# Kernel tuning notes

Measured on AMD Instinct MI355X. Metric: run time of the kernel, lower is better.

## Reference

```python
import jax, jax.numpy as jnp
import numpy as np

B, T, S0 = 8, 4, 4096
D_MODEL, H, D, R, RANK = 2048, 16, 128, 64, 512
C = D - R  # content dim = 64


def _rope(x, positions):
    # x: [B, H, T, R]; rotate-half style RoPE as in the torch module
    half = x.shape[-1] // 2
    inv_freq = 1.0 / (10000.0 ** (jnp.arange(half, dtype=jnp.float32) / half))
    freqs = positions.astype(jnp.float32)[:, None] * inv_freq[None, :]  # [T, half]
    cos = jnp.cos(freqs)[None, None].astype(x.dtype)
    sin = jnp.sin(freqs)[None, None].astype(x.dtype)
    x1, x2 = x[..., :half], x[..., half:]
    return jnp.concatenate([x1 * cos - x2 * sin, x1 * sin + x2 * cos], axis=-1)


def setup_inputs() -> dict:
    key = jax.random.key(0)
    ks = jax.random.split(key, 9)
    s = 0.02
    return {
        "x": jax.random.normal(ks[0], (B, T, D_MODEL), jnp.float32),
        "cache_c_kv": jax.random.normal(ks[1], (B, S0, RANK), jnp.float32),
        "cache_k_rope": jax.random.normal(ks[2], (B, S0, H, R), jnp.float32),
        "w_q": jax.random.normal(ks[3], (D_MODEL, H * C), jnp.float32) * s,
        "w_q_rope": jax.random.normal(ks[4], (D_MODEL, H * R), jnp.float32) * s,
        "w_kv_down": jax.random.normal(ks[5], (D_MODEL, RANK), jnp.float32) * s,
        "w_kv_up": jax.random.normal(ks[6], (RANK, H * D), jnp.float32) * s,
        "w_k_rope": jax.random.normal(ks[7], (D_MODEL, H * R), jnp.float32) * s,
        "w_out": jax.random.normal(ks[8], (H * D, D_MODEL), jnp.float32) * s,
    }


def reference(x, cache_c_kv, cache_k_rope, w_q, w_q_rope, w_kv_down, w_kv_up, w_k_rope, w_out):
    cache_len = cache_c_kv.shape[1]
    positions = jnp.arange(cache_len, cache_len + T)

    # queries
    q_content = (x @ w_q).reshape(B, T, H, C).transpose(0, 2, 1, 3)        # [B,H,T,C]
    q_rope = (x @ w_q_rope).reshape(B, T, H, R).transpose(0, 2, 1, 3)      # [B,H,T,R]
    q_rope = _rope(q_rope, positions)
    q = jnp.concatenate([q_content, q_rope], axis=-1)                       # [B,H,T,D]

    # new compressed kv + rope keys, append to cache
    c_kv_new = x @ w_kv_down                                                # [B,T,RANK]
    k_rope_new = (x @ w_k_rope).reshape(B, T, H, R).transpose(0, 2, 1, 3)
    k_rope_new = _rope(k_rope_new, positions).transpose(0, 2, 1, 3)         # [B,T,H,R]
    c_kv = jnp.concatenate([cache_c_kv, c_kv_new], axis=1)                  # [B,S,RANK]
    k_rope = jnp.concatenate([cache_k_rope, k_rope_new], axis=1)            # [B,S,H,R]

    # decompress full cache every step (the expensive MLA pattern)
    S = c_kv.shape[1]
    kv = (c_kv @ w_kv_up).reshape(B, S, H, D)                               # [B,S,H,D]
    k_content = kv[..., :C].transpose(0, 2, 1, 3)                           # [B,H,S,C]
    v = kv.transpose(0, 2, 1, 3)                                            # [B,H,S,D]
    k = jnp.concatenate([k_content, k_rope.transpose(0, 2, 1, 3)], axis=-1) # [B,H,S,D]

    # kv_cache present => is_prefill False => no causal mask (faithful to source)
    scale = 1.0 / jnp.sqrt(jnp.asarray(D, dtype=q.dtype))
    scores = jnp.einsum('bhtd,bhsd->bhts', q, k) * scale
    attn = jax.nn.softmax(scores, axis=-1)
    out = jnp.einsum('bhts,bhsd->bhtd', attn, v)                            # [B,H,T,D]
    out = out.transpose(0, 2, 1, 3).reshape(B, T, H * D)
    return out @ w_out                                                       # [B,T,D_MODEL]
```

## Files before the change

### kernel.cpp

```cpp
#include <hip/hip_runtime.h>
#include <hip/hip_fp16.h>
#include <cmath>

#define BB 8
#define TT 4
#define HH 16
#define DDIM 128
#define RRDIM 64
#define CCDIM 64
#define RANKC 512
#define DMODEL 2048
#define S0C 4096
#define NQ 64
#define HD 2048
#define NACT 3584
#define NSC 65
#define NG 17
#define SPAD 4160
#define SCALE_ATT 0.08838834764831845f

typedef __attribute__((ext_vector_type(8))) short bf16x8;
typedef __attribute__((ext_vector_type(4))) float f32x4;
typedef unsigned short ushortT;

#define AIDX(row, kk) ((row)*132 + (((row)>>2)<<2) + (kk))

static __device__ __forceinline__ unsigned short f2bf(float x) {
  unsigned u = __float_as_uint(x);
  u += 0x7FFFu + ((u >> 16) & 1u);
  return (unsigned short)(u >> 16);
}
static __device__ __forceinline__ unsigned pk2(float a, float b) {
  return (unsigned)f2bf(a) | ((unsigned)f2bf(b) << 16);
}

__global__ __launch_bounds__(256) void k_front(const float* __restrict__ A,
                                               const float* __restrict__ w0,
                                               const float* __restrict__ w1,
                                               const float* __restrict__ w2,
                                               const float* __restrict__ w3,
                                               const float* __restrict__ cckv,
                                               float* __restrict__ part,
                                               ushortT* __restrict__ ckvB,
                                               ushortT* __restrict__ ckvT,
                                               float* __restrict__ rctab) {
  __shared__ float shf[4352];
  const int tid = threadIdx.x;
  const int bx = blockIdx.x;
  if (bx < 448) {
    const int cb = bx % 28;
    const int k0 = (bx / 28) * 128;
    const float* W; int N, lc0, off;
    if (cb < 8)       { W = w0; N = 1024; lc0 = cb * 128;        off = 0; }
    else if (cb < 16) { W = w1; N = 1024; lc0 = (cb - 8) * 128;  off = 1024; }
    else if (cb < 20) { W = w2; N = 512;  lc0 = (cb - 16) * 128; off = 2048; }
    else              { W = w3; N = 1024; lc0 = (cb - 20) * 128; off = 2560; }
    {
      const int row = tid >> 3;
      const int kseg = (tid & 7) * 16;
      const float4* s4 = reinterpret_cast<const float4*>(A + (size_t)row * DMODEL + k0 + kseg);
      float4 v0 = s4[0], v1 = s4[1], v2 = s4[2], v3 = s4[3];
      *reinterpret_cast<float4*>(&shf[AIDX(row, kseg)])      = v0;
      *reinterpret_cast<float4*>(&shf[AIDX(row, kseg + 4)])  = v1;
      *reinterpret_cast<float4*>(&shf[AIDX(row, kseg + 8)])  = v2;
      *reinterpret_cast<float4*>(&shf[AIDX(row, kseg + 12)]) = v3;
    }
    __syncthreads();
    const int cg = tid & 31;
    const int rg = tid >> 5;
    float acc[4][4];
    #pragma unroll
    for (int r = 0; r < 4; ++r)
      #pragma unroll
      for (int c = 0; c < 4; ++c) acc[r][c] = 0.f;
    #pragma unroll 4
    for (int kk = 0; kk < 128; ++kk) {
      const float4 w4 = *reinterpret_cast<const float4*>(W + (size_t)(k0 + kk) * N + lc0 + cg * 4);
      const float wv[4] = {w4.x, w4.y, w4.z, w4.w};
      #pragma unroll
      for (int r = 0; r < 4; ++r) {
        const float av = shf[AIDX(rg * 4 + r, kk)];
        #pragma unroll
        for (int c = 0; c < 4; ++c) acc[r][c] = fmaf(av, wv[c], acc[r][c]);
      }
    }
    #pragma unroll
    for (int r = 0; r < 4; ++r) {
      float4 o = make_float4(acc[r][0], acc[r][1], acc[r][2], acc[r][3]);
      *reinterpret_cast<float4*>(part + ((size_t)(bx / 28) * 32 + rg * 4 + r) * NACT + off + lc0 + cg * 4) = o;
    }
  } else if (bx < 960) {
    ushortT* tlds = reinterpret_cast<ushortT*>(shf);
    const int idx = bx - 448;
    const int b = idx >> 6, c = idx & 63;
    const float* src = cckv + ((size_t)b * S0C + c * 64) * RANKC;
    ushortT* dstB = ckvB + ((size_t)(b * NSC + c) * 64) * RANKC;
    ushortT* dstT = ckvT + ((size_t)(b * NSC + c) * RANKC) * 64;
    const int s = tid >> 2, rq = tid & 3;
    const int rloc = tid >> 1, shalf = (tid & 1) * 32;
    for (int slab = 0; slab < 4; ++slab) {
      const int r0 = slab * 128;
      unsigned pk_arr[16];
      #pragma unroll
      for (int i = 0; i < 8; ++i) {
        const float4 v = *reinterpret_cast<const float4*>(src + (size_t)s * RANKC + r0 + rq * 32 + i * 4);
        pk_arr[2 * i]     = pk2(v.x, v.y);
        pk_arr[2 * i + 1] = pk2(v.z, v.w);
        *reinterpret_cast<uint2*>(&tlds[s * 136 + rq * 32 + i * 4]) =
            make_uint2(pk_arr[2 * i], pk_arr[2 * i + 1]);
      }
      {
        uint4* db = reinterpret_cast<uint4*>(dstB + (size_t)s * RANKC + r0 + rq * 32);
        db[0] = make_uint4(pk_arr[0], pk_arr[1], pk_arr[2], pk_arr[3]);
        db[1] = make_uint4(pk_arr[4], pk_arr[5], pk_arr[6], pk_arr[7]);
        db[2] = make_uint4(pk_arr[8], pk_arr[9], pk_arr[10], pk_arr[11]);
        db[3] = make_uint4(pk_arr[12], pk_arr[13], pk_arr[14], pk_arr[15]);
      }
      __syncthreads();
      unsigned pkv[16];
      #pragma unroll
      for (int k = 0; k < 16; ++k) {
        const unsigned t0 = tlds[(shalf + 2 * k)     * 136 + rloc];
        const unsigned t1 = tlds[(shalf + 2 * k + 1) * 136 + rloc];
        pkv[k] = t0 | (t1 << 16);
      }
      uint4* d = reinterpret_cast<uint4*>(dstT + ((size_t)(r0 + rloc)) * 64 + shalf);
      d[0] = make_uint4(pkv[0], pkv[1], pkv[2], pkv[3]);
      d[1] = make_uint4(pkv[4], pkv[5], pkv[6], pkv[7]);
      d[2] = make_uint4(pkv[8], pkv[9], pkv[10], pkv[11]);
      d[3] = make_uint4(pkv[12], pkv[13], pkv[14], pkv[15]);
      __syncthreads();
    }
  } else {
    const int b = bx - 960;
    const uint4 z = make_uint4(0, 0, 0, 0);
    uint4* p = reinterpret_cast<uint4*>(ckvT + ((size_t)(b * NSC + 64) * RANKC) * 64);
    for (int i = tid; i < 4096; i += 256) p[i] = z;
    uint4* q = reinterpret_cast<uint4*>(ckvB + (((size_t)(b * NSC + 64) * 64) + 4) * RANKC);
    for (int i = tid; i < 3840; i += 256) q[i] = z;
    if (bx == 960 && tid < 128) {
      const int t = tid >> 5, j = tid & 31;
      const double fr = (double)(S0C + t) * pow(10000.0, -(double)j / 32.0);
      rctab[t * 32 + j]       = (float)cos(fr);
      rctab[128 + t * 32 + j] = (float)sin(fr);
    }
  }
}

__global__ __launch_bounds__(256) void k_mid(const float* __restrict__ part0,
                                             const float* __restrict__ cache_kr,
                                             const float* __restrict__ wup,
                                             const float* __restrict__ rctab,
                                             ushortT* __restrict__ qlat,
                                             ushortT* __restrict__ ckvB,
                                             ushortT* __restrict__ ckvT,
                                             __half* __restrict__ rs) {
  __shared__ float smid[2176];
  const int tid = threadIdx.x;
  const int bx = blockIdx.x;
  if (bx < 1152) {
    const int bh = bx / 9, sy = bx % 9;
    const int b = bh >> 4, h = bh & 15;
    float* raw_q = smid;
    float* raw_k = smid + 256;
    float* qr_l  = smid + 512;
    float* kr_l  = smid + 768;
    {
      const int t = tid >> 6, j = tid & 63;
      const size_t rowoff = (size_t)(b * TT + t) * NACT;
      float sq = 0.f, sk = 0.f;
      #pragma unroll 4
      for (int ks = 0; ks < 16; ++ks) {
        const float* pp = part0 + (size_t)ks * (32 * NACT) + rowoff;
        sq += pp[1024 + h * 64 + j];
        sk += pp[2560 + h * 64 + j];
      }
      raw_q[t * 64 + j] = sq;
      raw_k[t * 64 + j] = sk;
    }
    __syncthreads();
    {
      const int t = tid >> 6, j = tid & 63;
      const int j2 = j & 31;
      const float cs = rctab[t * 32 + j2];
      const float sn = rctab[128 + t * 32 + j2];
      const float qa = raw_q[t * 64 + j], qp = raw_q[t * 64 + (j ^ 32)];
      const float ka = raw_k[t * 64 + j], kp = raw_k[t * 64 + (j ^ 32)];
      float qv, kv;
      if (j < 32) { qv = qa * cs - qp * sn; kv = ka * cs - kp * sn; }
      else        { qv = qp * sn + qa * cs; kv = kp * sn + ka * cs; }
      qr_l[t * 64 + j] = qv * SCALE_ATT;
      kr_l[t * 64 + j] = kv;
    }
    __syncthreads();
    const int ql = tid & 3;
    float4 qf[4][4];
    #pragma unroll
    for (int t = 0; t < 4; ++t)
      #pragma unroll
      for (int u = 0; u < 4; ++u)
        qf[t][u] = *reinterpret_cast<const float4*>(&qr_l[t * 64 + ql * 16 + u * 4]);
    const int s0 = sy * 512;
    #pragma unroll 2
    for (int pass = 0; pass < 8; ++pass) {
      const int s = s0 + pass * 64 + (tid >> 2);
      if (s < 4100) {
        float p[4] = {0.f, 0.f, 0.f, 0.f};
        const float* krow = (s < S0C)
            ? cache_kr + (((size_t)b * S0C + s) * HH + h) * RRDIM
            : &kr_l[(s - S0C) * 64];
        #pragma unroll
        for (int u = 0; u < 4; ++u) {
          const float4 kv = *reinterpret_cast<const float4*>(krow + ql * 16 + u * 4);
          #pragma unroll
          for (int t = 0; t < 4; ++t)
            p[t] += kv.x * qf[t][u].x + kv.y * qf[t][u].y
                  + kv.z * qf[t][u].z + kv.w * qf[t][u].w;
        }
        #pragma unroll
        for (int t = 0; t < 4; ++t) {
          p[t] += __shfl_xor(p[t], 1, 4);
          p[t] += __shfl_xor(p[t], 2, 4);
        }
        rs[((size_t)bh * 4 + ql) * SPAD + s] = __float2half(p[ql]);
      }
    }
  } else if (bx < 1216) {
    const int lx = bx - 1152;
    const int h = lx & 15;
    const int r0 = (lx >> 4) * 128;
    float* a_s = smid;
    {
      const int bt = tid >> 3;
      const int c8 = (tid & 7) * 8;
      float v[8] = {0.f,0.f,0.f,0.f,0.f,0.f,0.f,0.f};
      #pragma unroll 4
      for (int ks = 0; ks < 16; ++ks) {
        const float4* pp = reinterpret_cast<const float4*>(
            part0 + (size_t)ks * (32 * NACT) + (size_t)bt * NACT + h * CCDIM + c8);
        const float4 x0 = pp[0], x1 = pp[1];
        v[0]+=x0.x; v[1]+=x0.y; v[2]+=x0.z; v[3]+=x0.w;
        v[4]+=x1.x; v[5]+=x1.y; v[6]+=x1.z; v[7]+=x1.w;
      }
      #pragma unroll
      for (int u = 0; u < 8; ++u) a_s[bt * 68 + c8 + u] = v[u];
    }
    __syncthreads();
    const int r = tid & 127;
    const int bth = tid >> 7;
    const float* wrow = wup + (size_t)(r0 + r) * HD + h * DDIM;
    float4 wreg[16];
    #pragma unroll
    for (int u = 0; u < 16; ++u)
      wreg[u] = *reinterpret_cast<const float4*>(wrow + u * 4);
    float acc[16];
    #pragma unroll
    for (int i = 0; i < 16; ++i) acc[i] = 0.f;
    #pragma unroll
    for (int u = 0; u < 16; ++u) {
      #pragma unroll
      for (int i = 0; i < 16; ++i) {
        const float4 av = *reinterpret_cast<const float4*>(&a_s[(bth * 16 + i) * 68 + u * 4]);
        acc[i] = fmaf(av.x, wreg[u].x, acc[i]);
        acc[i] = fmaf(av.y, wreg[u].y, acc[i]);
        acc[i] = fmaf(av.z, wreg[u].z, acc[i]);
        acc[i] = fmaf(av.w, wreg[u].w, acc[i]);
      }
    }
    #pragma unroll
    for (int i = 0; i < 16; ++i) {
      const int bt = bth * 16 + i;
      const int b = bt >> 2, t = bt & 3;
      qlat[((size_t)(b * NQ) + h * TT + t) * RANKC + r0 + r] = f2bf(acc[i]);
    }
  } else {
    const int g = (bx - 1216) * 256 + tid;
    const int r = g & 511;
    const int bt = g >> 9;
    const int b = bt >> 2, t = bt & 3;
    float s = 0.f;
    #pragma unroll 4
    for (int ks = 0; ks < 16; ++ks)
      s += part0[(size_t)ks * (32 * NACT) + (size_t)bt * NACT + 2048 + r];
    const ushortT bv = f2bf(s);
    ckvB[(((size_t)(b * NSC + 64) * 64) + t) * RANKC + r] = bv;
    ckvT[(((size_t)(b * NSC + 64) * RANKC) + r) * 64 + t] = bv;
  }
}

__global__ __launch_bounds__(256) void k_score(
    const ushortT* __restrict__ ckvB, const ushortT* __restrict__ qlat,
    const __half* __restrict__ rs, float* __restrict__ ml,
    ushortT* __restrict__ Pg) {
  __shared__ ushortT PL[64 * 72];
  const int tid = threadIdx.x;
  const int wv = tid >> 6;
  const int lane = tid & 63;
  const int lm = lane & 15, lg = lane >> 4;
  const int b = blockIdx.x, chunk = blockIdx.y;
  const int qbase = wv * 16;
  const int scnt = (chunk < 64) ? 64 : TT;
  const ushortT* bsrc = ckvB + ((size_t)(b * NSC + chunk) * 64) * RANKC;

  const ushortT* qrow = qlat + ((size_t)b * NQ + qbase + lm) * RANKC + lg * 8;
  bf16x8 qa[16];
  #pragma unroll
  for (int ks = 0; ks < 16; ++ks)
    qa[ks] = *reinterpret_cast<const bf16x8*>(qrow + ks * 32);

  f32x4 acc[4];
  #pragma unroll
  for (int st = 0; st < 4; ++st) acc[st] = (f32x4){0.f, 0.f, 0.f, 0.f};
  #pragma unroll
  for (int ks = 0; ks < 16; ++ks) {
    #pragma unroll
    for (int st = 0; st < 4; ++st) {
      const bf16x8 bf = *reinterpret_cast<const bf16x8*>(
          bsrc + (size_t)(st * 16 + lm) * RANKC + ks * 32 + lg * 8);
      acc[st] = __builtin_amdgcn_mfma_f32_16x16x32_bf16(qa[ks], bf, acc[st], 0, 0, 0);
    }
  }

  #pragma unroll
  for (int reg = 0; reg < 4; ++reg) {
    const int qi = qbase + lg * 4 + reg;
    const __half* rp = rs + (((size_t)(b * HH) + (qi >> 2)) * TT + (qi & 3)) * SPAD + chunk * 64;
    float vvv[4];
    float mx = -1e30f;
    #pragma unroll
    for (int st = 0; st < 4; ++st) {
      const int sl = st * 16 + lm;
      const float val = (sl < scnt)
          ? fmaf(acc[st][reg], SCALE_ATT, __half2float(rp[sl]))
          : -1e30f;
      vvv[st] = val;
      mx = fmaxf(mx, val);
    }
    #pragma unroll
    for (int off = 1; off < 16; off <<= 1) mx = fmaxf(mx, __shfl_xor(mx, off, 16));
    float sum = 0.f;
    #pragma unroll
    for (int st = 0; st < 4; ++st) {
      const float p = __expf(vvv[st] - mx);
      vvv[st] = p;
      sum += p;
    }
    #pragma unroll
    for (int off = 1; off < 16; off <<= 1) sum += __shfl_xor(sum, off, 16);
    #pragma unroll
    for (int st = 0; st < 4; ++st)
      PL[(qbase + lg * 4 + reg) * 72 + st * 16 + lm] = f2bf(vvv[st]);
    if (lm == 0) {
      const size_t mb = (((size_t)b * NSC + chunk) * NQ + qi) * 2;
      ml[mb] = mx; ml[mb + 1] = sum;
    }
  }
  __syncthreads();
  {
    const int row = tid >> 2, seg = (tid & 3) * 16;
    const uint4* sp = reinterpret_cast<const uint4*>(&PL[row * 72 + seg]);
    uint4* dp = reinterpret_cast<uint4*>(
        Pg + ((size_t)(b * NSC + chunk) * NQ + row) * 64 + seg);
    dp[0] = sp[0]; dp[1] = sp[1];
  }
}

__global__ __launch_bounds__(256) void k_pv(
    const ushortT* __restrict__ ckvT, const ushortT* __restrict__ Pg,
    const float* __restrict__ ml, float* __restrict__ olat,
    float* __restrict__ mlg) {
  const int tid = threadIdx.x;
  const int wv = tid >> 6;
  const int lane = tid & 63;
  const int lm = lane & 15, lg = lane >> 4;
  const int b = blockIdx.x, g = blockIdx.y, rg = blockIdx.z;
  const int qbase = wv * 16;
  const int nc = (g < 16) ? 4 : 1;
  const int c0 = (g < 16) ? g * 4 : 64;

  float m_cl = -1e30f, l_cl = 0.f;
  if (lg < nc) {
    const size_t mb = (((size_t)b * NSC + c0 + lg) * NQ + qbase + lm) * 2;
    m_cl = ml[mb]; l_cl = ml[mb + 1];
  }
  float mg = fmaxf(m_cl, __shfl_xor(m_cl, 16));
  mg = fmaxf(mg, __shfl_xor(mg, 32));
  const float wgt = (lg < nc) ? __expf(m_cl - mg) : 0.f;
  float la = l_cl * wgt;
  la += __shfl_xor(la, 16);
  la += __shfl_xor(la, 32);
  if (rg == 0 && lg == 0) {
    const size_t gb = (((size_t)b * NG + g) * NQ + qbase + lm) * 2;
    mlg[gb] = mg; mlg[gb + 1] = la;
  }
  float wf[4][4];
  #pragma unroll
  for (int c = 0; c < 4; ++c)
    #pragma unroll
    for (int reg = 0; reg < 4; ++reg)
      wf[c][reg] = __shfl(wgt, c * 16 + lg * 4 + reg);

  f32x4 OACC[8];
  #pragma unroll
  for (int nt = 0; nt < 8; ++nt) OACC[nt] = (f32x4){0.f, 0.f, 0.f, 0.f};

  for (int c = 0; c < nc; ++c) {
    const ushortT* pb = Pg + ((size_t)(b * NSC + c0 + c) * NQ + qbase + lm) * 64 + lg * 8;
    const bf16x8 pa0 = *reinterpret_cast<const bf16x8*>(pb);
    const bf16x8 pa1 = *reinterpret_cast<const bf16x8*>(pb + 32);
    const ushortT* vb = ckvT + (((size_t)(b * NSC + c0 + c) * RANKC) + rg * 128 + lm) * 64 + lg * 8;
    f32x4 a2[8];
    #pragma unroll
    for (int nt = 0; nt < 8; ++nt) a2[nt] = (f32x4){0.f, 0.f, 0.f, 0.f};
    #pragma unroll
    for (int nt = 0; nt < 8; ++nt) {
      const bf16x8 b0 = *reinterpret_cast<const bf16x8*>(vb + (size_t)nt * 16 * 64);
      const bf16x8 b1 = *reinterpret_cast<const bf16x8*>(vb + (size_t)nt * 16 * 64 + 32);
      a2[nt] = __builtin_amdgcn_mfma_f32_16x16x32_bf16(pa0, b0, a2[nt], 0, 0, 0);
      a2[nt] = __builtin_amdgcn_mfma_f32_16x16x32_bf16(pa1, b1, a2[nt], 0, 0, 0);
    }
    const f32x4 wv4 = {wf[c][0], wf[c][1], wf[c][2], wf[c][3]};
    #pragma unroll
    for (int nt = 0; nt < 8; ++nt) OACC[nt] += wv4 * a2[nt];
  }

  const size_t obase = ((size_t)(b * NG + g) * NQ) * RANKC;
  #pragma unroll
  for (int nt = 0; nt < 8; ++nt)
    #pragma unroll
    for (int reg = 0; reg < 4; ++reg)
      olat[obase + (size_t)(qbase + lg * 4 + reg) * RANKC + rg * 128 + nt * 16 + lm] = OACC[nt][reg];
}

__global__ __launch_bounds__(512) void k_combF(const float* __restrict__ mlg,
                                               const float* __restrict__ olat,
                                               const float* __restrict__ wup,
                                               float* __restrict__ ohead,
                                               float* __restrict__ out) {
  __shared__ float wrow[4][20];
  __shared__ float att_lds[4][516];
  __shared__ float red[4][4][32][4];
  const int h = blockIdx.x, b = blockIdx.y;
  const int tid = threadIdx.x;
  {
    const int t = tid >> 7, col = tid & 127;
    out[(size_t)(b * TT + t) * HD + h * DDIM + col] = 0.f;
  }
  const int wave = tid >> 6;
  const int i = wave >> 1;
  const int rhalf = wave & 1;
  const int rl = tid & 63;
  const int qi = h * TT + i;
  float m1 = -1e30f, l1 = 0.f;
  if (rl < NG) {
    const size_t base = (((size_t)b * NG + rl) * NQ + qi) * 2;
    m1 = mlg[base]; l1 = mlg[base + 1];
  }
  float M = m1;
  #pragma unroll
  for (int off = 1; off < 64; off <<= 1) M = fmaxf(M, __shfl_xor(M, off));
  float L = (rl < NG) ? l1 * __expf(m1 - M) : 0.f;
  #pragma unroll
  for (int off = 1; off < 64; off <<= 1) L += __shfl_xor(L, off);
  const float invL = 1.0f / L;
  if (rl < NG) wrow[i][rl] = __expf(m1 - M) * invL;
  __syncthreads();
  const int r0 = rhalf * 256 + rl * 4;
  {
    float o0 = 0.f, o1 = 0.f, o2 = 0.f, o3 = 0.f;
    for (int c = 0; c < NG; ++c) {
      const float w = wrow[i][c];
      const float4 v = *reinterpret_cast<const float4*>(
          olat + (((size_t)b * NG + c) * NQ + qi) * RANKC + r0);
      o0 = fmaf(v.x, w, o0); o1 = fmaf(v.y, w, o1);
      o2 = fmaf(v.z, w, o2); o3 = fmaf(v.w, w, o3);
    }
    *reinterpret_cast<float4*>(&att_lds[i][r0]) = make_float4(o0, o1, o2, o3);
  }
  __syncthreads();
  const int t = tid >> 7;
  const int rq = (tid >> 5) & 3;
  const int c4 = tid & 31;
  const float* wb = wup + (size_t)h * DDIM + c4 * 4;
  float a0 = 0.f, a1 = 0.f, a2 = 0.f, a3 = 0.f;
  const int rbeg = rq * 128;
  #pragma unroll 4
  for (int rr = 0; rr < 128; ++rr) {
    const int r = rbeg + rr;
    const float4 w4 = *reinterpret_cast<const float4*>(wb + (size_t)r * HD);
    const float a = att_lds[t][r];
    a0 = fmaf(a, w4.x, a0); a1 = fmaf(a, w4.y, a1);
    a2 = fmaf(a, w4.z, a2); a3 = fmaf(a, w4.w, a3);
  }
  *reinterpret_cast<float4*>(&red[rq][t][c4][0]) = make_float4(a0, a1, a2, a3);
  __syncthreads();
  if (tid < 128) {
    const int t2 = tid >> 5, c42 = tid & 31;
    float4 s = make_float4(0.f, 0.f, 0.f, 0.f);
    #pragma unroll
    for (int q = 0; q < 4; ++q) {
      const float4 v = *reinterpret_cast<const float4*>(&red[q][t2][c42][0]);
      s.x += v.x; s.y += v.y; s.z += v.z; s.w += v.w;
    }
    *reinterpret_cast<float4*>(&ohead[(size_t)(b * TT + t2) * HD + h * DDIM + c42 * 4]) = s;
  }
}

__global__ __launch_bounds__(256) void k_projA(const float* __restrict__ A,
                                               const float* __restrict__ W,
                                               float* __restrict__ out) {
  __shared__ float a_lds[4352];
  const int tid = threadIdx.x;
  const int c0 = blockIdx.x * 128;
  const int k0 = blockIdx.y * 128;
  {
    const int row = tid >> 3;
    const int kseg = (tid & 7) * 16;
    const float4* s4 = reinterpret_cast<const float4*>(A + (size_t)row * DMODEL + k0 + kseg);
    float4 v0 = s4[0], v1 = s4[1], v2 = s4[2], v3 = s4[3];
    *reinterpret_cast<float4*>(&a_lds[AIDX(row, kseg)])      = v0;
    *reinterpret_cast<float4*>(&a_lds[AIDX(row, kseg + 4)])  = v1;
    *reinterpret_cast<float4*>(&a_lds[AIDX(row, kseg + 8)])  = v2;
    *reinterpret_cast<float4*>(&a_lds[AIDX(row, kseg + 12)]) = v3;
  }
  __syncthreads();
  const int cg = tid & 31;
  const int rg = tid >> 5;
  float acc[4][4];
  #pragma unroll
  for (int r = 0; r < 4; ++r)
    #pragma unroll
    for (int c = 0; c < 4; ++c) acc[r][c] = 0.f;
  #pragma unroll 4
  for (int kk = 0; kk < 128; ++kk) {
    const float4 w4 = *reinterpret_cast<const float4*>(W + (size_t)(k0 + kk) * HD + c0 + cg * 4);
    const float wv[4] = {w4.x, w4.y, w4.z, w4.w};
    #pragma unroll
    for (int r = 0; r < 4; ++r) {
      const float av = a_lds[AIDX(rg * 4 + r, kk)];
      #pragma unroll
      for (int c = 0; c < 4; ++c) acc[r][c] = fmaf(av, wv[c], acc[r][c]);
    }
  }
  #pragma unroll
  for (int r = 0; r < 4; ++r)
    #pragma unroll
    for (int c = 0; c < 4; ++c)
      unsafeAtomicAdd(&out[(size_t)(rg * 4 + r) * HD + c0 + cg * 4 + c], acc[r][c]);
}

extern "C" void kernel_launch(void* const* d_in, const int* in_sizes, int n_in,
                              void* d_out, int out_size, void* d_ws, size_t ws_size,
                              hipStream_t stream) {
  const float* x     = (const float*)d_in[0];
  const float* cckv  = (const float*)d_in[1];
  const float* ckr   = (const float*)d_in[2];
  const float* w_q   = (const float*)d_in[3];
  const float* w_qr  = (const float*)d_in[4];
  const float* w_kvd = (const float*)d_in[5];
  const float* w_kvu = (const float*)d_in[6];
  const float* w_kr  = (const float*)d_in[7];
  const float* w_out = (const float*)d_in[8];
  float* out = (float*)d_out;
  float* ws = (float*)d_ws;

  size_t off = 0;
  ushortT* qlat   = (ushortT*)(ws + off); off += 131072;
  float* mlb      = ws + off; off += (size_t)BB * NSC * NQ * 2;
  float* mlgb     = ws + off; off += (size_t)BB * NG * NQ * 2;
  float* ohead    = ws + off; off += 65536;
  float* rctab    = ws + off; off += 256;
  __half* rsb     = (__half*)(ws + off); off += 1064960;
  ushortT* ckvB   = (ushortT*)(ws + off); off += 8519680;
  ushortT* ckvT   = (ushortT*)(ws + off); off += 8519680;
  ushortT* Pgb    = (ushortT*)(ws + off); off += 1064960;
  float* regB  = ws + off;
  float* part0 = regB;
  float* olat  = regB;

  k_front<<<dim3(968), 256, 0, stream>>>(x, w_q, w_qr, w_kvd, w_kr, cckv, part0, ckvB, ckvT, rctab);
  k_mid<<<dim3(1280), 256, 0, stream>>>(part0, ckr, w_kvu, rctab, qlat, ckvB, ckvT, rsb);
  k_score<<<dim3(BB, NSC), 256, 0, stream>>>(ckvB, qlat, rsb, mlb, Pgb);
  k_pv<<<dim3(BB, NG, 4), 256, 0, stream>>>(ckvT, Pgb, mlb, olat, mlgb);
  k_combF<<<dim3(16, 8), 512, 0, stream>>>(mlgb, olat, w_kvu, ohead, out);
  k_projA<<<dim3(16, 16), 256, 0, stream>>>(ohead, w_out, out);
}
```

Before: 210.1 us.

## Raise parallelism across MLA stages with atomic split-K reductions and finer grids

The front projection now accumulates its K-split partial sums with atomic adds into a zeroed activation buffer instead of writing 16 partial slabs that later stages summed. The cache conversion work is split into one block per 128-column slab, and the mid, pv and combine kernels are launched with more, smaller blocks; the combine kernel splits the rank dimension across blocks and accumulates into ohead atomically. The aim is to fill more CUs and cut redundant partial-sum reads, at the cost of extra memsets, atomic traffic and non-deterministic summation order.

```diff
diff --git a/kernel.cpp b/kernel.cpp
--- a/kernel.cpp
+++ b/kernel.cpp
@@ -40,7 +40,7 @@
                                                const float* __restrict__ w2,
                                                const float* __restrict__ w3,
                                                const float* __restrict__ cckv,
-                                               float* __restrict__ part,
+                                               float* __restrict__ act,
                                                ushortT* __restrict__ ckvB,
                                                ushortT* __restrict__ ckvT,
                                                float* __restrict__ rctab) {
@@ -85,60 +85,57 @@
       }
     }
     #pragma unroll
-    for (int r = 0; r < 4; ++r) {
-      float4 o = make_float4(acc[r][0], acc[r][1], acc[r][2], acc[r][3]);
-      *reinterpret_cast<float4*>(part + ((size_t)(bx / 28) * 32 + rg * 4 + r) * NACT + off + lc0 + cg * 4) = o;
-    }
-  } else if (bx < 960) {
+    for (int r = 0; r < 4; ++r)
+      #pragma unroll
+      for (int c = 0; c < 4; ++c)
+        unsafeAtomicAdd(&act[(size_t)(rg * 4 + r) * NACT + off + lc0 + cg * 4 + c], acc[r][c]);
+  } else if (bx < 2496) {
     ushortT* tlds = reinterpret_cast<ushortT*>(shf);
     const int idx = bx - 448;
-    const int b = idx >> 6, c = idx & 63;
+    const int b = idx >> 8, c = (idx >> 2) & 63, slab = idx & 3;
+    const int r0 = slab * 128;
     const float* src = cckv + ((size_t)b * S0C + c * 64) * RANKC;
     ushortT* dstB = ckvB + ((size_t)(b * NSC + c) * 64) * RANKC;
     ushortT* dstT = ckvT + ((size_t)(b * NSC + c) * RANKC) * 64;
     const int s = tid >> 2, rq = tid & 3;
     const int rloc = tid >> 1, shalf = (tid & 1) * 32;
-    for (int slab = 0; slab < 4; ++slab) {
-      const int r0 = slab * 128;
-      unsigned pk_arr[16];
-      #pragma unroll
-      for (int i = 0; i < 8; ++i) {
-        const float4 v = *reinterpret_cast<const float4*>(src + (size_t)s * RANKC + r0 + rq * 32 + i * 4);
-        pk_arr[2 * i]     = pk2(v.x, v.y);
-        pk_arr[2 * i + 1] = pk2(v.z, v.w);
-        *reinterpret_cast<uint2*>(&tlds[s * 136 + rq * 32 + i * 4]) =
-            make_uint2(pk_arr[2 * i], pk_arr[2 * i + 1]);
-      }
-      {
-        uint4* db = reinterpret_cast<uint4*>(dstB + (size_t)s * RANKC + r0 + rq * 32);
-        db[0] = make_uint4(pk_arr[0], pk_arr[1], pk_arr[2], pk_arr[3]);
-        db[1] = make_uint4(pk_arr[4], pk_arr[5], pk_arr[6], pk_arr[7]);
-        db[2] = make_uint4(pk_arr[8], pk_arr[9], pk_arr[10], pk_arr[11]);
-        db[3] = make_uint4(pk_arr[12], pk_arr[13], pk_arr[14], pk_arr[15]);
-      }
-      __syncthreads();
-      unsigned pkv[16];
-      #pragma unroll
-      for (int k = 0; k < 16; ++k) {
-        const unsigned t0 = tlds[(shalf + 2 * k)     * 136 + rloc];
-        const unsigned t1 = tlds[(shalf + 2 * k + 1) * 136 + rloc];
-        pkv[k] = t0 | (t1 << 16);
-      }
-      uint4* d = reinterpret_cast<uint4*>(dstT + ((size_t)(r0 + rloc)) * 64 + shalf);
-      d[0] = make_uint4(pkv[0], pkv[1], pkv[2], pkv[3]);
-      d[1] = make_uint4(pkv[4], pkv[5], pkv[6], pkv[7]);
-      d[2] = make_uint4(pkv[8], pkv[9], pkv[10], pkv[11]);
-      d[3] = make_uint4(pkv[12], pkv[13], pkv[14], pkv[15]);
-      __syncthreads();
-    }
+    unsigned pk_arr[16];
+    #pragma unroll
+    for (int i = 0; i < 8; ++i) {
+      const float4 v = *reinterpret_cast<const float4*>(src + (size_t)s * RANKC + r0 + rq * 32 + i * 4);
+      pk_arr[2 * i]     = pk2(v.x, v.y);
+      pk_arr[2 * i + 1] = pk2(v.z, v.w);
+      *reinterpret_cast<uint2*>(&tlds[s * 136 + rq * 32 + i * 4]) =
+          make_uint2(pk_arr[2 * i], pk_arr[2 * i + 1]);
+    }
+    {
+      uint4* db = reinterpret_cast<uint4*>(dstB + (size_t)s * RANKC + r0 + rq * 32);
+      db[0] = make_uint4(pk_arr[0], pk_arr[1], pk_arr[2], pk_arr[3]);
+      db[1] = make_uint4(pk_arr[4], pk_arr[5], pk_arr[6], pk_arr[7]);
+      db[2] = make_uint4(pk_arr[8], pk_arr[9], pk_arr[10], pk_arr[11]);
+      db[3] = make_uint4(pk_arr[12], pk_arr[13], pk_arr[14], pk_arr[15]);
+    }
+    __syncthreads();
+    unsigned pkv[16];
+    #pragma unroll
+    for (int k = 0; k < 16; ++k) {
+      const unsigned t0 = tlds[(shalf + 2 * k)     * 136 + rloc];
+      const unsigned t1 = tlds[(shalf + 2 * k + 1) * 136 + rloc];
+      pkv[k] = t0 | (t1 << 16);
+    }
+    uint4* d = reinterpret_cast<uint4*>(dstT + ((size_t)(r0 + rloc)) * 64 + shalf);
+    d[0] = make_uint4(pkv[0], pkv[1], pkv[2], pkv[3]);
+    d[1] = make_uint4(pkv[4], pkv[5], pkv[6], pkv[7]);
+    d[2] = make_uint4(pkv[8], pkv[9], pkv[10], pkv[11]);
+    d[3] = make_uint4(pkv[12], pkv[13], pkv[14], pkv[15]);
   } else {
-    const int b = bx - 960;
+    const int b = bx - 2496;
     const uint4 z = make_uint4(0, 0, 0, 0);
     uint4* p = reinterpret_cast<uint4*>(ckvT + ((size_t)(b * NSC + 64) * RANKC) * 64);
     for (int i = tid; i < 4096; i += 256) p[i] = z;
     uint4* q = reinterpret_cast<uint4*>(ckvB + (((size_t)(b * NSC + 64) * 64) + 4) * RANKC);
     for (int i = tid; i < 3840; i += 256) q[i] = z;
-    if (bx == 960 && tid < 128) {
+    if (bx == 2496 && tid < 128) {
       const int t = tid >> 5, j = tid & 31;
       const double fr = (double)(S0C + t) * pow(10000.0, -(double)j / 32.0);
       rctab[t * 32 + j]       = (float)cos(fr);
@@ -147,7 +144,7 @@
   }
 }
 
-__global__ __launch_bounds__(256) void k_mid(const float* __restrict__ part0,
+__global__ __launch_bounds__(256) void k_mid(const float* __restrict__ act,
                                              const float* __restrict__ cache_kr,
                                              const float* __restrict__ wup,
                                              const float* __restrict__ rctab,
@@ -158,25 +155,18 @@
   __shared__ float smid[2176];
   const int tid = threadIdx.x;
   const int bx = blockIdx.x;
-  if (bx < 1152) {
-    const int bh = bx / 9, sy = bx % 9;
+  if (bx < 2304) {
+    const int bh = bx / 18, sy = bx % 18;
     const int b = bh >> 4, h = bh & 15;
     float* raw_q = smid;
     float* raw_k = smid + 256;
     float* qr_l  = smid + 512;
     float* kr_l  = smid + 768;
-    {
+    if (tid < 256) {
       const int t = tid >> 6, j = tid & 63;
       const size_t rowoff = (size_t)(b * TT + t) * NACT;
-      float sq = 0.f, sk = 0.f;
-      #pragma unroll 4
-      for (int ks = 0; ks < 16; ++ks) {
-        const float* pp = part0 + (size_t)ks * (32 * NACT) + rowoff;
-        sq += pp[1024 + h * 64 + j];
-        sk += pp[2560 + h * 64 + j];
-      }
-      raw_q[t * 64 + j] = sq;
-      raw_k[t * 64 + j] = sk;
+      raw_q[t * 64 + j] = act[rowoff + 1024 + h * 64 + j];
+      raw_k[t * 64 + j] = act[rowoff + 2560 + h * 64 + j];
     }
     __syncthreads();
     {
@@ -200,9 +190,9 @@
       #pragma unroll
       for (int u = 0; u < 4; ++u)
         qf[t][u] = *reinterpret_cast<const float4*>(&qr_l[t * 64 + ql * 16 + u * 4]);
-    const int s0 = sy * 512;
+    const int s0 = sy * 256;
     #pragma unroll 2
-    for (int pass = 0; pass < 8; ++pass) {
+    for (int pass = 0; pass < 4; ++pass) {
       const int s = s0 + pass * 64 + (tid >> 2);
       if (s < 4100) {
         float p[4] = {0.f, 0.f, 0.f, 0.f};
@@ -225,25 +215,20 @@
         rs[((size_t)bh * 4 + ql) * SPAD + s] = __float2half(p[ql]);
       }
     }
-  } else if (bx < 1216) {
-    const int lx = bx - 1152;
+  } else if (bx < 2368) {
+    const int lx = bx - 2304;
     const int h = lx & 15;
     const int r0 = (lx >> 4) * 128;
     float* a_s = smid;
     {
       const int bt = tid >> 3;
       const int c8 = (tid & 7) * 8;
-      float v[8] = {0.f,0.f,0.f,0.f,0.f,0.f,0.f,0.f};
-      #pragma unroll 4
-      for (int ks = 0; ks < 16; ++ks) {
-        const float4* pp = reinterpret_cast<const float4*>(
-            part0 + (size_t)ks * (32 * NACT) + (size_t)bt * NACT + h * CCDIM + c8);
-        const float4 x0 = pp[0], x1 = pp[1];
-        v[0]+=x0.x; v[1]+=x0.y; v[2]+=x0.z; v[3]+=x0.w;
-        v[4]+=x1.x; v[5]+=x1.y; v[6]+=x1.z; v[7]+=x1.w;
-      }
-      #pragma unroll
-      for (int u = 0; u < 8; ++u) a_s[bt * 68 + c8 + u] = v[u];
+      const float4* pp = reinterpret_cast<const float4*>(act + (size_t)bt * NACT + h * CCDIM + c8);
+      const float4 x0 = pp[0], x1 = pp[1];
+      a_s[bt * 68 + c8 + 0] = x0.x; a_s[bt * 68 + c8 + 1] = x0.y;
+      a_s[bt * 68 + c8 + 2] = x0.z; a_s[bt * 68 + c8 + 3] = x0.w;
+      a_s[bt * 68 + c8 + 4] = x1.x; a_s[bt * 68 + c8 + 5] = x1.y;
+      a_s[bt * 68 + c8 + 6] = x1.z; a_s[bt * 68 + c8 + 7] = x1.w;
     }
     __syncthreads();
     const int r = tid & 127;
@@ -274,14 +259,11 @@
       qlat[((size_t)(b * NQ) + h * TT + t) * RANKC + r0 + r] = f2bf(acc[i]);
     }
   } else {
-    const int g = (bx - 1216) * 256 + tid;
+    const int g = (bx - 2368) * 256 + tid;
     const int r = g & 511;
     const int bt = g >> 9;
     const int b = bt >> 2, t = bt & 3;
-    float s = 0.f;
-    #pragma unroll 4
-    for (int ks = 0; ks < 16; ++ks)
-      s += part0[(size_t)ks * (32 * NACT) + (size_t)bt * NACT + 2048 + r];
+    const float s = act[(size_t)bt * NACT + 2048 + r];
     const ushortT bv = f2bf(s);
     ckvB[(((size_t)(b * NSC + 64) * 64) + t) * RANKC + r] = bv;
     ckvT[(((size_t)(b * NSC + 64) * RANKC) + r) * 64 + t] = bv;
@@ -400,20 +382,20 @@
     for (int reg = 0; reg < 4; ++reg)
       wf[c][reg] = __shfl(wgt, c * 16 + lg * 4 + reg);
 
-  f32x4 OACC[8];
-  #pragma unroll
-  for (int nt = 0; nt < 8; ++nt) OACC[nt] = (f32x4){0.f, 0.f, 0.f, 0.f};
+  f32x4 OACC[4];
+  #pragma unroll
+  for (int nt = 0; nt < 4; ++nt) OACC[nt] = (f32x4){0.f, 0.f, 0.f, 0.f};
 
   for (int c = 0; c < nc; ++c) {
     const ushortT* pb = Pg + ((size_t)(b * NSC + c0 + c) * NQ + qbase + lm) * 64 + lg * 8;
     const bf16x8 pa0 = *reinterpret_cast<const bf16x8*>(pb);
     const bf16x8 pa1 = *reinterpret_cast<const bf16x8*>(pb + 32);
-    const ushortT* vb = ckvT + (((size_t)(b * NSC + c0 + c) * RANKC) + rg * 128 + lm) * 64 + lg * 8;
-    f32x4 a2[8];
-    #pragma unroll
-    for (int nt = 0; nt < 8; ++nt) a2[nt] = (f32x4){0.f, 0.f, 0.f, 0.f};
-    #pragma unroll
-    for (int nt = 0; nt < 8; ++nt) {
+    const ushortT* vb = ckvT + (((size_t)(b * NSC + c0 + c) * RANKC) + rg * 64 + lm) * 64 + lg * 8;
+    f32x4 a2[4];
+    #pragma unroll
+    for (int nt = 0; nt < 4; ++nt) a2[nt] = (f32x4){0.f, 0.f, 0.f, 0.f};
+    #pragma unroll
+    for (int nt = 0; nt < 4; ++nt) {
       const bf16x8 b0 = *reinterpret_cast<const bf16x8*>(vb + (size_t)nt * 16 * 64);
       const bf16x8 b1 = *reinterpret_cast<const bf16x8*>(vb + (size_t)nt * 16 * 64 + 32);
       a2[nt] = __builtin_amdgcn_mfma_f32_16x16x32_bf16(pa0, b0, a2[nt], 0, 0, 0);
@@ -421,34 +403,27 @@
     }
     const f32x4 wv4 = {wf[c][0], wf[c][1], wf[c][2], wf[c][3]};
     #pragma unroll
-    for (int nt = 0; nt < 8; ++nt) OACC[nt] += wv4 * a2[nt];
+    for (int nt = 0; nt < 4; ++nt) OACC[nt] += wv4 * a2[nt];
   }
 
   const size_t obase = ((size_t)(b * NG + g) * NQ) * RANKC;
   #pragma unroll
-  for (int nt = 0; nt < 8; ++nt)
+  for (int nt = 0; nt < 4; ++nt)
     #pragma unroll
     for (int reg = 0; reg < 4; ++reg)
-      olat[obase + (size_t)(qbase + lg * 4 + reg) * RANKC + rg * 128 + nt * 16 + lm] = OACC[nt][reg];
-}
-
-__global__ __launch_bounds__(512) void k_combF(const float* __restrict__ mlg,
+      olat[obase + (size_t)(qbase + lg * 4 + reg) * RANKC + rg * 64 + nt * 16 + lm] = OACC[nt][reg];
+}
+
+__global__ __launch_bounds__(256) void k_combF(const float* __restrict__ mlg,
                                                const float* __restrict__ olat,
                                                const float* __restrict__ wup,
-                                               float* __restrict__ ohead,
-                                               float* __restrict__ out) {
+                                               float* __restrict__ ohead) {
   __shared__ float wrow[4][20];
-  __shared__ float att_lds[4][516];
-  __shared__ float red[4][4][32][4];
-  const int h = blockIdx.x, b = blockIdx.y;
+  __shared__ float red[2][4][32][4];
+  __shared__ float att_l[4][128];
+  const int h = blockIdx.x, b = blockIdx.y, rq = blockIdx.z;
   const int tid = threadIdx.x;
-  {
-    const int t = tid >> 7, col = tid & 127;
-    out[(size_t)(b * TT + t) * HD + h * DDIM + col] = 0.f;
-  }
-  const int wave = tid >> 6;
-  const int i = wave >> 1;
-  const int rhalf = wave & 1;
+  const int i = tid >> 6;
   const int rl = tid & 63;
   const int qi = h * TT + i;
   float m1 = -1e30f, l1 = 0.f;
@@ -465,44 +440,49 @@
   const float invL = 1.0f / L;
   if (rl < NG) wrow[i][rl] = __expf(m1 - M) * invL;
   __syncthreads();
-  const int r0 = rhalf * 256 + rl * 4;
   {
+    const int ch = tid >> 7;
+    const int t = (tid >> 5) & 3;
+    const int p32 = tid & 31;
+    const int qit = h * TT + t;
+    const int cbeg = ch ? 9 : 0, cend = ch ? NG : 9;
     float o0 = 0.f, o1 = 0.f, o2 = 0.f, o3 = 0.f;
-    for (int c = 0; c < NG; ++c) {
-      const float w = wrow[i][c];
+    for (int c = cbeg; c < cend; ++c) {
+      const float w = wrow[t][c];
       const float4 v = *reinterpret_cast<const float4*>(
-          olat + (((size_t)b * NG + c) * NQ + qi) * RANKC + r0);
+          olat + (((size_t)b * NG + c) * NQ + qit) * RANKC + rq * 128 + p32 * 4);
       o0 = fmaf(v.x, w, o0); o1 = fmaf(v.y, w, o1);
       o2 = fmaf(v.z, w, o2); o3 = fmaf(v.w, w, o3);
     }
-    *reinterpret_cast<float4*>(&att_lds[i][r0]) = make_float4(o0, o1, o2, o3);
-  }
-  __syncthreads();
-  const int t = tid >> 7;
-  const int rq = (tid >> 5) & 3;
-  const int c4 = tid & 31;
-  const float* wb = wup + (size_t)h * DDIM + c4 * 4;
-  float a0 = 0.f, a1 = 0.f, a2 = 0.f, a3 = 0.f;
-  const int rbeg = rq * 128;
-  #pragma unroll 4
-  for (int rr = 0; rr < 128; ++rr) {
-    const int r = rbeg + rr;
-    const float4 w4 = *reinterpret_cast<const float4*>(wb + (size_t)r * HD);
-    const float a = att_lds[t][r];
-    a0 = fmaf(a, w4.x, a0); a1 = fmaf(a, w4.y, a1);
-    a2 = fmaf(a, w4.z, a2); a3 = fmaf(a, w4.w, a3);
-  }
-  *reinterpret_cast<float4*>(&red[rq][t][c4][0]) = make_float4(a0, a1, a2, a3);
+    *reinterpret_cast<float4*>(&red[ch][t][p32][0]) = make_float4(o0, o1, o2, o3);
+  }
   __syncthreads();
   if (tid < 128) {
-    const int t2 = tid >> 5, c42 = tid & 31;
-    float4 s = make_float4(0.f, 0.f, 0.f, 0.f);
-    #pragma unroll
-    for (int q = 0; q < 4; ++q) {
-      const float4 v = *reinterpret_cast<const float4*>(&red[q][t2][c42][0]);
-      s.x += v.x; s.y += v.y; s.z += v.z; s.w += v.w;
-    }
-    *reinterpret_cast<float4*>(&ohead[(size_t)(b * TT + t2) * HD + h * DDIM + c42 * 4]) = s;
+    const int t = tid >> 5, p32 = tid & 31;
+    const float4 v0 = *reinterpret_cast<const float4*>(&red[0][t][p32][0]);
+    const float4 v1 = *reinterpret_cast<const float4*>(&red[1][t][p32][0]);
+    *reinterpret_cast<float4*>(&att_l[t][p32 * 4]) =
+        make_float4(v0.x + v1.x, v0.y + v1.y, v0.z + v1.z, v0.w + v1.w);
+  }
+  __syncthreads();
+  {
+    const int rhalf = tid >> 7;
+    const int t = (tid >> 5) & 3;
+    const int c4 = tid & 31;
+    const float* wb = wup + (size_t)(rq * 128 + rhalf * 64) * HD + h * DDIM + c4 * 4;
+    float a0 = 0.f, a1 = 0.f, a2 = 0.f, a3 = 0.f;
+    #pragma unroll 4
+    for (int rr = 0; rr < 64; ++rr) {
+      const float4 w4 = *reinterpret_cast<const float4*>(wb + (size_t)rr * HD);
+      const float a = att_l[t][rhalf * 64 + rr];
+      a0 = fmaf(a, w4.x, a0); a1 = fmaf(a, w4.y, a1);
+      a2 = fmaf(a, w4.z, a2); a3 = fmaf(a, w4.w, a3);
+    }
+    float* dst = &ohead[(size_t)(b * TT + t) * HD + h * DDIM + c4 * 4];
+    unsafeAtomicAdd(dst + 0, a0);
+    unsafeAtomicAdd(dst + 1, a1);
+    unsafeAtomicAdd(dst + 2, a2);
+    unsafeAtomicAdd(dst + 3, a3);
   }
 }
 
@@ -565,6 +545,7 @@
   float* ws = (float*)d_ws;
 
   size_t off = 0;
+  float* act      = ws + off; off += 32ull * NACT;
   ushortT* qlat   = (ushortT*)(ws + off); off += 131072;
   float* mlb      = ws + off; off += (size_t)BB * NSC * NQ * 2;
   float* mlgb     = ws + off; off += (size_t)BB * NG * NQ * 2;
@@ -574,14 +555,16 @@
   ushortT* ckvB   = (ushortT*)(ws + off); off += 8519680;
   ushortT* ckvT   = (ushortT*)(ws + off); off += 8519680;
   ushortT* Pgb    = (ushortT*)(ws + off); off += 1064960;
-  float* regB  = ws + off;
-  float* part0 = regB;
-  float* olat  = regB;
-
-  k_front<<<dim3(968), 256, 0, stream>>>(x, w_q, w_qr, w_kvd, w_kr, cckv, part0, ckvB, ckvT, rctab);
-  k_mid<<<dim3(1280), 256, 0, stream>>>(part0, ckr, w_kvu, rctab, qlat, ckvB, ckvT, rsb);
+  float* olat     = ws + off;
+
+  hipMemsetAsync(act, 0, 32ull * NACT * sizeof(float), stream);
+  hipMemsetAsync(ohead, 0, 65536 * sizeof(float), stream);
+  hipMemsetAsync(out, 0, (size_t)out_size * sizeof(float), stream);
+
+  k_front<<<dim3(2504), 256, 0, stream>>>(x, w_q, w_qr, w_kvd, w_kr, cckv, act, ckvB, ckvT, rctab);
+  k_mid<<<dim3(2432), 256, 0, stream>>>(act, ckr, w_kvu, rctab, qlat, ckvB, ckvT, rsb);
   k_score<<<dim3(BB, NSC), 256, 0, stream>>>(ckvB, qlat, rsb, mlb, Pgb);
-  k_pv<<<dim3(BB, NG, 4), 256, 0, stream>>>(ckvT, Pgb, mlb, olat, mlgb);
-  k_combF<<<dim3(16, 8), 512, 0, stream>>>(mlgb, olat, w_kvu, ohead, out);
+  k_pv<<<dim3(BB, NG, 8), 256, 0, stream>>>(ckvT, Pgb, mlb, olat, mlgb);
+  k_combF<<<dim3(16, 8, 4), 256, 0, stream>>>(mlgb, olat, w_kvu, ohead);
   k_projA<<<dim3(16, 16), 256, 0, stream>>>(ohead, w_out, out);
 }
```

Result: slower. 226.7 us (+7.9%).

## Fuse score/softmax and PV kernels into one attention kernel via LDS

Applied to the files above, without the earlier changes.

Merges the separate score+local-softmax kernel and the PV kernel into a single k_att kernel. Each block handles a group of up to four chunks for half the queries; each wave computes scores for one chunk, keeps the probabilities and per-chunk max/sum in shared memory, and then each wave does PV for a 128-wide rank slice. This drops the global Pg/ml round trip and one launch. The trade-off is a smaller grid (272 blocks instead of 520+544), idle waves in the tail group during the score phase, and each block re-reading Q and both cache layouts for its chunks.

```diff
diff --git a/kernel.cpp b/kernel.cpp
--- a/kernel.cpp
+++ b/kernel.cpp
@@ -288,148 +288,134 @@
   }
 }
 
-__global__ __launch_bounds__(256) void k_score(
-    const ushortT* __restrict__ ckvB, const ushortT* __restrict__ qlat,
-    const __half* __restrict__ rs, float* __restrict__ ml,
-    ushortT* __restrict__ Pg) {
-  __shared__ ushortT PL[64 * 72];
+__global__ __launch_bounds__(256) void k_att(
+    const ushortT* __restrict__ ckvB, const ushortT* __restrict__ ckvT,
+    const ushortT* __restrict__ qlat, const __half* __restrict__ rs,
+    float* __restrict__ olat, float* __restrict__ mlg) {
+  __shared__ ushortT PL[4][32 * 72];
+  __shared__ float mlS[4][2][32];
+  __shared__ float wS[4][32];
   const int tid = threadIdx.x;
   const int wv = tid >> 6;
   const int lane = tid & 63;
   const int lm = lane & 15, lg = lane >> 4;
-  const int b = blockIdx.x, chunk = blockIdx.y;
-  const int qbase = wv * 16;
-  const int scnt = (chunk < 64) ? 64 : TT;
-  const ushortT* bsrc = ckvB + ((size_t)(b * NSC + chunk) * 64) * RANKC;
-
-  const ushortT* qrow = qlat + ((size_t)b * NQ + qbase + lm) * RANKC + lg * 8;
-  bf16x8 qa[16];
-  #pragma unroll
-  for (int ks = 0; ks < 16; ++ks)
-    qa[ks] = *reinterpret_cast<const bf16x8*>(qrow + ks * 32);
-
-  f32x4 acc[4];
-  #pragma unroll
-  for (int st = 0; st < 4; ++st) acc[st] = (f32x4){0.f, 0.f, 0.f, 0.f};
-  #pragma unroll
-  for (int ks = 0; ks < 16; ++ks) {
-    #pragma unroll
-    for (int st = 0; st < 4; ++st) {
-      const bf16x8 bf = *reinterpret_cast<const bf16x8*>(
-          bsrc + (size_t)(st * 16 + lm) * RANKC + ks * 32 + lg * 8);
-      acc[st] = __builtin_amdgcn_mfma_f32_16x16x32_bf16(qa[ks], bf, acc[st], 0, 0, 0);
-    }
-  }
-
-  #pragma unroll
-  for (int reg = 0; reg < 4; ++reg) {
-    const int qi = qbase + lg * 4 + reg;
-    const __half* rp = rs + (((size_t)(b * HH) + (qi >> 2)) * TT + (qi & 3)) * SPAD + chunk * 64;
-    float vvv[4];
-    float mx = -1e30f;
-    #pragma unroll
-    for (int st = 0; st < 4; ++st) {
-      const int sl = st * 16 + lm;
-      const float val = (sl < scnt)
-          ? fmaf(acc[st][reg], SCALE_ATT, __half2float(rp[sl]))
-          : -1e30f;
-      vvv[st] = val;
-      mx = fmaxf(mx, val);
-    }
-    #pragma unroll
-    for (int off = 1; off < 16; off <<= 1) mx = fmaxf(mx, __shfl_xor(mx, off, 16));
-    float sum = 0.f;
-    #pragma unroll
-    for (int st = 0; st < 4; ++st) {
-      const float p = __expf(vvv[st] - mx);
-      vvv[st] = p;
-      sum += p;
-    }
-    #pragma unroll
-    for (int off = 1; off < 16; off <<= 1) sum += __shfl_xor(sum, off, 16);
-    #pragma unroll
-    for (int st = 0; st < 4; ++st)
-      PL[(qbase + lg * 4 + reg) * 72 + st * 16 + lm] = f2bf(vvv[st]);
-    if (lm == 0) {
-      const size_t mb = (((size_t)b * NSC + chunk) * NQ + qi) * 2;
-      ml[mb] = mx; ml[mb + 1] = sum;
-    }
-  }
-  __syncthreads();
-  {
-    const int row = tid >> 2, seg = (tid & 3) * 16;
-    const uint4* sp = reinterpret_cast<const uint4*>(&PL[row * 72 + seg]);
-    uint4* dp = reinterpret_cast<uint4*>(
-        Pg + ((size_t)(b * NSC + chunk) * NQ + row) * 64 + seg);
-    dp[0] = sp[0]; dp[1] = sp[1];
-  }
-}
-
-__global__ __launch_bounds__(256) void k_pv(
-    const ushortT* __restrict__ ckvT, const ushortT* __restrict__ Pg,
-    const float* __restrict__ ml, float* __restrict__ olat,
-    float* __restrict__ mlg) {
-  const int tid = threadIdx.x;
-  const int wv = tid >> 6;
-  const int lane = tid & 63;
-  const int lm = lane & 15, lg = lane >> 4;
-  const int b = blockIdx.x, g = blockIdx.y, rg = blockIdx.z;
-  const int qbase = wv * 16;
+  const int g = blockIdx.x, b = blockIdx.y, qh = blockIdx.z;
+  const int qbase = qh * 32;
   const int nc = (g < 16) ? 4 : 1;
   const int c0 = (g < 16) ? g * 4 : 64;
 
-  float m_cl = -1e30f, l_cl = 0.f;
-  if (lg < nc) {
-    const size_t mb = (((size_t)b * NSC + c0 + lg) * NQ + qbase + lm) * 2;
-    m_cl = ml[mb]; l_cl = ml[mb + 1];
-  }
-  float mg = fmaxf(m_cl, __shfl_xor(m_cl, 16));
-  mg = fmaxf(mg, __shfl_xor(mg, 32));
-  const float wgt = (lg < nc) ? __expf(m_cl - mg) : 0.f;
-  float la = l_cl * wgt;
-  la += __shfl_xor(la, 16);
-  la += __shfl_xor(la, 32);
-  if (rg == 0 && lg == 0) {
-    const size_t gb = (((size_t)b * NG + g) * NQ + qbase + lm) * 2;
+  if (wv < nc) {
+    const int myc = c0 + wv;
+    const int scnt = (myc < 64) ? 64 : TT;
+    const ushortT* bsrc = ckvB + ((size_t)(b * NSC + myc) * 64) * RANKC;
+    const ushortT* qrow = qlat + ((size_t)b * NQ + qbase + lm) * RANKC + lg * 8;
+    f32x4 acc[2][4];
+    #pragma unroll
+    for (int qm = 0; qm < 2; ++qm)
+      #pragma unroll
+      for (int st = 0; st < 4; ++st) acc[qm][st] = (f32x4){0.f, 0.f, 0.f, 0.f};
+    #pragma unroll
+    for (int ks = 0; ks < 16; ++ks) {
+      const bf16x8 qa0 = *reinterpret_cast<const bf16x8*>(qrow + ks * 32);
+      const bf16x8 qa1 = *reinterpret_cast<const bf16x8*>(qrow + 16 * RANKC + ks * 32);
+      #pragma unroll
+      for (int st = 0; st < 4; ++st) {
+        const bf16x8 bf = *reinterpret_cast<const bf16x8*>(
+            bsrc + (size_t)(st * 16 + lm) * RANKC + ks * 32 + lg * 8);
+        acc[0][st] = __builtin_amdgcn_mfma_f32_16x16x32_bf16(qa0, bf, acc[0][st], 0, 0, 0);
+        acc[1][st] = __builtin_amdgcn_mfma_f32_16x16x32_bf16(qa1, bf, acc[1][st], 0, 0, 0);
+      }
+    }
+    #pragma unroll
+    for (int qm = 0; qm < 2; ++qm) {
+      #pragma unroll
+      for (int reg = 0; reg < 4; ++reg) {
+        const int ql = qm * 16 + lg * 4 + reg;
+        const int qi = qbase + ql;
+        const __half* rp = rs + (((size_t)(b * HH) + (qi >> 2)) * TT + (qi & 3)) * SPAD + myc * 64;
+        float vvv[4];
+        float mx = -1e30f;
+        #pragma unroll
+        for (int st = 0; st < 4; ++st) {
+          const int sl = st * 16 + lm;
+          const float val = (sl < scnt)
+              ? fmaf(acc[qm][st][reg], SCALE_ATT, __half2float(rp[sl]))
+              : -1e30f;
+          vvv[st] = val;
+          mx = fmaxf(mx, val);
+        }
+        #pragma unroll
+        for (int off = 1; off < 16; off <<= 1) mx = fmaxf(mx, __shfl_xor(mx, off, 16));
+        float sum = 0.f;
+        #pragma unroll
+        for (int st = 0; st < 4; ++st) {
+          const float p = __expf(vvv[st] - mx);
+          vvv[st] = p;
+          sum += p;
+        }
+        #pragma unroll
+        for (int off = 1; off < 16; off <<= 1) sum += __shfl_xor(sum, off, 16);
+        #pragma unroll
+        for (int st = 0; st < 4; ++st)
+          PL[wv][ql * 72 + st * 16 + lm] = f2bf(vvv[st]);
+        if (lm == 0) { mlS[wv][0][ql] = mx; mlS[wv][1][ql] = sum; }
+      }
+    }
+  }
+  __syncthreads();
+
+  if (tid < 32) {
+    const int q = tid;
+    float mg = -1e30f;
+    for (int c = 0; c < nc; ++c) mg = fmaxf(mg, mlS[c][0][q]);
+    float la = 0.f;
+    for (int c = 0; c < nc; ++c) {
+      const float w = __expf(mlS[c][0][q] - mg);
+      wS[c][q] = w;
+      la = fmaf(mlS[c][1][q], w, la);
+    }
+    const size_t gb = (((size_t)b * NG + g) * NQ + qbase + q) * 2;
     mlg[gb] = mg; mlg[gb + 1] = la;
   }
-  float wf[4][4];
+  __syncthreads();
+
+  const int rg = wv;
+  f32x4 OACC[2][8];
   #pragma unroll
-  for (int c = 0; c < 4; ++c)
-    #pragma unroll
-    for (int reg = 0; reg < 4; ++reg)
-      wf[c][reg] = __shfl(wgt, c * 16 + lg * 4 + reg);
-
-  f32x4 OACC[8];
-  #pragma unroll
-  for (int nt = 0; nt < 8; ++nt) OACC[nt] = (f32x4){0.f, 0.f, 0.f, 0.f};
-
+  for (int qm = 0; qm < 2; ++qm)
+    #pragma unroll
+    for (int rn = 0; rn < 8; ++rn) OACC[qm][rn] = (f32x4){0.f, 0.f, 0.f, 0.f};
   for (int c = 0; c < nc; ++c) {
-    const ushortT* pb = Pg + ((size_t)(b * NSC + c0 + c) * NQ + qbase + lm) * 64 + lg * 8;
-    const bf16x8 pa0 = *reinterpret_cast<const bf16x8*>(pb);
-    const bf16x8 pa1 = *reinterpret_cast<const bf16x8*>(pb + 32);
-    const ushortT* vb = ckvT + (((size_t)(b * NSC + c0 + c) * RANKC) + rg * 128 + lm) * 64 + lg * 8;
-    f32x4 a2[8];
-    #pragma unroll
-    for (int nt = 0; nt < 8; ++nt) a2[nt] = (f32x4){0.f, 0.f, 0.f, 0.f};
-    #pragma unroll
-    for (int nt = 0; nt < 8; ++nt) {
-      const bf16x8 b0 = *reinterpret_cast<const bf16x8*>(vb + (size_t)nt * 16 * 64);
-      const bf16x8 b1 = *reinterpret_cast<const bf16x8*>(vb + (size_t)nt * 16 * 64 + 32);
-      a2[nt] = __builtin_amdgcn_mfma_f32_16x16x32_bf16(pa0, b0, a2[nt], 0, 0, 0);
-      a2[nt] = __builtin_amdgcn_mfma_f32_16x16x32_bf16(pa1, b1, a2[nt], 0, 0, 0);
-    }
-    const f32x4 wv4 = {wf[c][0], wf[c][1], wf[c][2], wf[c][3]};
-    #pragma unroll
-    for (int nt = 0; nt < 8; ++nt) OACC[nt] += wv4 * a2[nt];
-  }
-
+    const bf16x8 pa00 = *reinterpret_cast<const bf16x8*>(&PL[c][lm * 72 + lg * 8]);
+    const bf16x8 pa01 = *reinterpret_cast<const bf16x8*>(&PL[c][lm * 72 + 32 + lg * 8]);
+    const bf16x8 pa10 = *reinterpret_cast<const bf16x8*>(&PL[c][(16 + lm) * 72 + lg * 8]);
+    const bf16x8 pa11 = *reinterpret_cast<const bf16x8*>(&PL[c][(16 + lm) * 72 + 32 + lg * 8]);
+    const f32x4 w0 = {wS[c][lg * 4 + 0], wS[c][lg * 4 + 1], wS[c][lg * 4 + 2], wS[c][lg * 4 + 3]};
+    const f32x4 w1 = {wS[c][16 + lg * 4 + 0], wS[c][16 + lg * 4 + 1],
+                      wS[c][16 + lg * 4 + 2], wS[c][16 + lg * 4 + 3]};
+    const ushortT* vb = ckvT + ((size_t)(b * NSC + c0 + c) * RANKC + rg * 128 + lm) * 64 + lg * 8;
+    #pragma unroll
+    for (int rn = 0; rn < 8; ++rn) {
+      const bf16x8 b0 = *reinterpret_cast<const bf16x8*>(vb + (size_t)rn * 16 * 64);
+      const bf16x8 b1 = *reinterpret_cast<const bf16x8*>(vb + (size_t)rn * 16 * 64 + 32);
+      f32x4 t0 = (f32x4){0.f, 0.f, 0.f, 0.f}, t1 = (f32x4){0.f, 0.f, 0.f, 0.f};
+      t0 = __builtin_amdgcn_mfma_f32_16x16x32_bf16(pa00, b0, t0, 0, 0, 0);
+      t0 = __builtin_amdgcn_mfma_f32_16x16x32_bf16(pa01, b1, t0, 0, 0, 0);
+      t1 = __builtin_amdgcn_mfma_f32_16x16x32_bf16(pa10, b0, t1, 0, 0, 0);
+      t1 = __builtin_amdgcn_mfma_f32_16x16x32_bf16(pa11, b1, t1, 0, 0, 0);
+      OACC[0][rn] += w0 * t0;
+      OACC[1][rn] += w1 * t1;
+    }
+  }
   const size_t obase = ((size_t)(b * NG + g) * NQ) * RANKC;
   #pragma unroll
-  for (int nt = 0; nt < 8; ++nt)
-    #pragma unroll
-    for (int reg = 0; reg < 4; ++reg)
-      olat[obase + (size_t)(qbase + lg * 4 + reg) * RANKC + rg * 128 + nt * 16 + lm] = OACC[nt][reg];
+  for (int qm = 0; qm < 2; ++qm)
+    #pragma unroll
+    for (int rn = 0; rn < 8; ++rn)
+      #pragma unroll
+      for (int reg = 0; reg < 4; ++reg)
+        olat[obase + (size_t)(qbase + qm * 16 + lg * 4 + reg) * RANKC + rg * 128 + rn * 16 + lm]
+            = OACC[qm][rn][reg];
 }
 
 __global__ __launch_bounds__(512) void k_combF(const float* __restrict__ mlg,
@@ -566,22 +552,19 @@
 
   size_t off = 0;
   ushortT* qlat   = (ushortT*)(ws + off); off += 131072;
-  float* mlb      = ws + off; off += (size_t)BB * NSC * NQ * 2;
   float* mlgb     = ws + off; off += (size_t)BB * NG * NQ * 2;
   float* ohead    = ws + off; off += 65536;
   float* rctab    = ws + off; off += 256;
   __half* rsb     = (__half*)(ws + off); off += 1064960;
   ushortT* ckvB   = (ushortT*)(ws + off); off += 8519680;
   ushortT* ckvT   = (ushortT*)(ws + off); off += 8519680;
-  ushortT* Pgb    = (ushortT*)(ws + off); off += 1064960;
   float* regB  = ws + off;
   float* part0 = regB;
   float* olat  = regB;
 
   k_front<<<dim3(968), 256, 0, stream>>>(x, w_q, w_qr, w_kvd, w_kr, cckv, part0, ckvB, ckvT, rctab);
   k_mid<<<dim3(1280), 256, 0, stream>>>(part0, ckr, w_kvu, rctab, qlat, ckvB, ckvT, rsb);
-  k_score<<<dim3(BB, NSC), 256, 0, stream>>>(ckvB, qlat, rsb, mlb, Pgb);
-  k_pv<<<dim3(BB, NG, 4), 256, 0, stream>>>(ckvT, Pgb, mlb, olat, mlgb);
+  k_att<<<dim3(NG, BB, 2), 256, 0, stream>>>(ckvB, ckvT, qlat, rsb, olat, mlgb);
   k_combF<<<dim3(16, 8), 512, 0, stream>>>(mlgb, olat, w_kvu, ohead, out);
   k_projA<<<dim3(16, 16), 256, 0, stream>>>(ohead, w_out, out);
 }
```

Result: faster. 194.6 us (median of 2 runs) (-7.4%).
